# Performance work log

Measured on AMD Instinct MI355X. Metric: run time of the kernel, lower is better.

## Reference

```python
import jax, jax.numpy as jnp
import numpy as np
import math

N = 50000   # nodes
E = 800000  # edges
D = 64      # in_feat_dim == out_feat_dim
T = 8       # num node types
R = 8       # num relations
SQRT_DK = math.sqrt(D)


def typed_matmul(x, W, types, num_types):
    """Row-wise x[i] @ W[types[i]] without materializing [E, D, D] gathered weights."""
    out = jnp.zeros((x.shape[0], W.shape[-1]), x.dtype)
    for t in range(num_types):
        out = out + jnp.where((types == t)[:, None], x @ W[t], 0.0)
    return out


def segment_softmax(score, index, num_segments):
    smax = jax.ops.segment_max(score, index, num_segments=num_segments)
    ex = jnp.exp(score - smax[index])
    ssum = jax.ops.segment_sum(ex, index, num_segments=num_segments)
    return ex / (ssum[index] + 1e-16)


def setup_inputs() -> dict:
    key = jax.random.key(0)
    ks = jax.random.split(key, 10)
    h = jax.random.normal(ks[0], (N, D), dtype=jnp.float32)
    adj = jax.random.randint(ks[1], (2, E), 0, N, dtype=jnp.int64)
    edge_type = jax.random.randint(ks[2], (E,), 0, R, dtype=jnp.int64)
    node_type = jax.random.randint(ks[3], (N,), 0, T, dtype=jnp.int64)
    k_weights = jax.random.uniform(ks[4], (T, D, D), dtype=jnp.float32)
    q_weights = jax.random.uniform(ks[5], (T, D, D), dtype=jnp.float32)
    v_weights = jax.random.uniform(ks[6], (T, D, D), dtype=jnp.float32)
    a_weights = jax.random.uniform(ks[7], (T, D, D), dtype=jnp.float32)
    relation_att = jax.random.uniform(ks[8], (R, D, D), dtype=jnp.float32)
    relation_msg = jax.random.uniform(ks[9], (R, D, D), dtype=jnp.float32)
    relation_pri = jnp.ones((R, 1), dtype=jnp.float32)
    skip = jnp.ones((T,), dtype=jnp.float32)
    return {
        "h": h, "adj": adj, "edge_type": edge_type, "node_type": node_type,
        "src_type": 0, "dst_type": 0,
        "k_weights": k_weights, "q_weights": q_weights, "v_weights": v_weights,
        "a_weights": a_weights, "relation_pri": relation_pri,
        "relation_att": relation_att, "relation_msg": relation_msg, "skip": skip,
    }


def reference(h, adj, edge_type, node_type, src_type, dst_type,
              k_weights, q_weights, v_weights, a_weights,
              relation_pri, relation_att, relation_msg, skip):
    src = adj[0]  # _j side (messages come from src)
    dst = adj[1]  # _i side (scatter/softmax index)

    # Node-type-indexed projections (done per node, then gathered per edge --
    # identical math to the per-edge bmm in the original).
    k_node = typed_matmul(h, k_weights, node_type, T)  # [N, D]
    q_node = typed_matmul(h, q_weights, node_type, T)
    v_node = typed_matmul(h, v_weights, node_type, T)

    # Relation-indexed per-edge transforms.
    k = typed_matmul(k_node[src], relation_att, edge_type, R)  # [E, D]
    v = typed_matmul(v_node[src], relation_msg, edge_type, R)  # [E, D]
    q = q_node[dst]                                            # [E, D]

    attn_score = jnp.sum(k * q, axis=1, keepdims=True) * relation_pri[edge_type] / SQRT_DK  # [E, 1]
    alpha = segment_softmax(attn_score, dst, N)  # edge softmax over incoming edges
    rst = v * alpha                              # [E, D]

    agg = jax.ops.segment_sum(rst, dst, num_segments=N)  # [N, D]

    # Update: node-type-indexed output transform scaled by sigmoid(skip[type]).
    trans_out = typed_matmul(agg, a_weights, node_type, T)
    alpha_skip = jax.nn.sigmoid(skip[node_type])
    return trans_out * alpha_skip[:, None]
```

## Files before the change

### kernel.cpp

```cpp
#include <hip/hip_runtime.h>
#include <math.h>

typedef float f32x4 __attribute__((ext_vector_type(4)));
typedef short bf16x8 __attribute__((ext_vector_type(8)));
typedef _Float16 f16x8 __attribute__((ext_vector_type(8)));
typedef _Float16 f16x4 __attribute__((ext_vector_type(4)));

#define D 64
#define TT 8
#define RR 8

#define SCAN_TPB 256
#define SCAN_CH 4
#define SCAN_ELEMS (SCAN_TPB * SCAN_CH)

#define HIST_CH 8
#define SCAT_CH 4
#define SCORE_XB 256
#define V2_XB 64
#define AGG_XB 256

__device__ __forceinline__ float bf2f(unsigned short u) {
    union { unsigned int i; float f; } x;
    x.i = ((unsigned int)u) << 16;
    return x.f;
}
__device__ __forceinline__ unsigned short f2bf(float f) {
    union { float f; unsigned int i; } x;
    x.f = f;
    unsigned int i = x.i;
    unsigned int r = (i + 0x7FFFu + ((i >> 16) & 1u)) >> 16;
    return (unsigned short)r;
}
struct BfPair { short hi; short lo; };
__device__ __forceinline__ BfPair split2(float x) {
    BfPair p;
    unsigned short h = f2bf(x);
    p.hi = (short)h;
    p.lo = (short)f2bf(x - bf2f(h));
    return p;
}
__device__ __forceinline__ void load_A_split(const float* __restrict__ p, bf16x8& ah, bf16x8& al) {
#pragma unroll
    for (int i = 0; i < 8; ++i) {
        BfPair s = split2(p[i]);
        ah[i] = s.hi; al[i] = s.lo;
    }
}
__device__ __forceinline__ void load_B_split(const float* __restrict__ W, int ks, int c, int lane,
                                             bf16x8& bh, bf16x8& bl) {
    int n = lane & 15, q = lane >> 4;
#pragma unroll
    for (int i = 0; i < 8; ++i) {
        BfPair s = split2(W[(ks * 32 + q * 8 + i) * 64 + c * 16 + n]);
        bh[i] = s.hi; bl[i] = s.lo;
    }
}
__device__ __forceinline__ void load_B_split_f16(const float* __restrict__ W, int ks, int c, int lane,
                                                 f16x8& bh, f16x8& bl) {
    int n = lane & 15, q = lane >> 4;
#pragma unroll
    for (int i = 0; i < 8; ++i) {
        float w = W[(ks * 32 + q * 8 + i) * 64 + c * 16 + n];
        _Float16 h = (_Float16)w;
        bh[i] = h;
        bl[i] = (_Float16)(w - (float)h);
    }
}
__device__ __forceinline__ f16x8 load_B_frag_f16(const float* __restrict__ W, int ks, int c, int lane) {
    int n = lane & 15, q = lane >> 4;
    f16x8 r;
#pragma unroll
    for (int i = 0; i < 8; ++i)
        r[i] = (_Float16)W[(ks * 32 + q * 8 + i) * 64 + c * 16 + n];
    return r;
}

#define MFMA16(a, b, c) __builtin_amdgcn_mfma_f32_16x16x32_bf16(a, b, c, 0, 0, 0)
#define MFMAH(a, b, c)  __builtin_amdgcn_mfma_f32_16x16x32_f16(a, b, c, 0, 0, 0)

#define SPLIT_MFMA_BODY(acc, A0h, A0l, A1h, A1l, Bh, Bl)          \
    _Pragma("unroll")                                             \
    for (int c = 0; c < 4; ++c) {                                 \
        acc[c] = MFMA16(A0h, Bh[0][c], acc[c]);                   \
        acc[c] = MFMA16(A0l, Bh[0][c], acc[c]);                   \
        acc[c] = MFMA16(A0h, Bl[0][c], acc[c]);                   \
        acc[c] = MFMA16(A1h, Bh[1][c], acc[c]);                   \
        acc[c] = MFMA16(A1l, Bh[1][c], acc[c]);                   \
        acc[c] = MFMA16(A1h, Bl[1][c], acc[c]);                   \
    }

__global__ void hist_kernel(const int* __restrict__ dst, const int* __restrict__ et,
                            const int* __restrict__ nt,
                            int* __restrict__ deg, int* __restrict__ tcnt, int* __restrict__ rcnt,
                            int* __restrict__ erank, int N, int E) {
    __shared__ int l_r[RR], l_t[TT];
    if (threadIdx.x < RR) l_r[threadIdx.x] = 0;
    if (threadIdx.x < TT) l_t[threadIdx.x] = 0;
    __syncthreads();
    const int stride = gridDim.x * blockDim.x;
    const int tid = blockIdx.x * blockDim.x + threadIdx.x;
#pragma unroll
    for (int i = 0; i < HIST_CH; ++i) {
        int e = tid + i * stride;
        if (e < E) {
            erank[e] = atomicAdd(&deg[dst[e]], 1);
            atomicAdd(&l_r[et[e]], 1);
        }
    }
#pragma unroll
    for (int i = 0; i < HIST_CH; ++i) {
        int n = tid + i * stride;
        if (n < N) atomicAdd(&l_t[nt[n]], 1);
    }
    __syncthreads();
    if (threadIdx.x < RR && l_r[threadIdx.x]) atomicAdd(&rcnt[threadIdx.x], l_r[threadIdx.x]);
    if (threadIdx.x < TT && l_t[threadIdx.x]) atomicAdd(&tcnt[threadIdx.x], l_t[threadIdx.x]);
}

__global__ void scan_sum_kernel(const int* __restrict__ deg, int* __restrict__ bsum, int N) {
    __shared__ int ws[SCAN_TPB / 64];
    int tid = threadIdx.x;
    int base = blockIdx.x * SCAN_ELEMS + tid * SCAN_CH;
    int s = 0;
#pragma unroll
    for (int i = 0; i < SCAN_CH; ++i) {
        int idx = base + i;
        if (idx < N) s += deg[idx];
    }
#pragma unroll
    for (int d = 32; d; d >>= 1) s += __shfl_xor(s, d, 64);
    if ((tid & 63) == 0) ws[tid >> 6] = s;
    __syncthreads();
    if (tid == 0) {
        int t = 0;
#pragma unroll
        for (int i = 0; i < SCAN_TPB / 64; ++i) t += ws[i];
        bsum[blockIdx.x] = t;
    }
}
__global__ void scan_out_kernel(const int* __restrict__ deg, const int* __restrict__ bsum, int nsb,
                                int* __restrict__ off, int N, int Etot,
                                const int* __restrict__ tcnt, int* __restrict__ toff, int* __restrict__ tcur,
                                const int* __restrict__ rcnt, int* __restrict__ roff, int* __restrict__ rcur) {
    __shared__ int ts[SCAN_TPB];
    __shared__ int bb;
    int tid = threadIdx.x;
    if (tid < 64) {
        int v = 0;
        if (nsb <= 64) {
            v = (tid < nsb && tid < blockIdx.x) ? bsum[tid] : 0;
#pragma unroll
            for (int d = 32; d; d >>= 1) v += __shfl_xor(v, d, 64);
        } else if (tid == 0) {
            for (int b = 0; b < blockIdx.x; ++b) v += bsum[b];
        }
        if (tid == 0) bb = v;
    }
    if (blockIdx.x == 0 && tid == 1) {
        int a = 0;
        for (int t = 0; t < TT; ++t) { toff[t] = a; tcur[t] = a; a += tcnt[t]; }
        toff[TT] = a;
        int b2 = 0;
        for (int r = 0; r < RR; ++r) { roff[r] = b2; rcur[r] = b2; b2 += rcnt[r]; }
        roff[RR] = b2;
        off[N] = Etot;
    }
    int base = blockIdx.x * SCAN_ELEMS + tid * SCAN_CH;
    int loc[SCAN_CH];
    int s = 0;
#pragma unroll
    for (int i = 0; i < SCAN_CH; ++i) {
        int idx = base + i;
        int v = (idx < N) ? deg[idx] : 0;
        loc[i] = v; s += v;
    }
    ts[tid] = s;
    __syncthreads();
    for (int sh = 1; sh < SCAN_TPB; sh <<= 1) {
        int v = (tid >= sh) ? ts[tid - sh] : 0;
        __syncthreads();
        ts[tid] += v;
        __syncthreads();
    }
    int run = bb + ((tid > 0) ? ts[tid - 1] : 0);
#pragma unroll
    for (int i = 0; i < SCAN_CH; ++i) {
        int idx = base + i;
        if (idx < N) { off[idx] = run; run += loc[i]; }
    }
}

__global__ void scatter_kernel(const int* __restrict__ src, const int* __restrict__ dst,
                               const int* __restrict__ et, const int* __restrict__ nt,
                               const int* __restrict__ offs, const int* __restrict__ erank,
                               int* __restrict__ tcur, int* __restrict__ rcur,
                               int* __restrict__ rsrc, int* __restrict__ rdst,
                               int* __restrict__ rdpos, int* __restrict__ nidx, int N, int E) {
    __shared__ int l_r[RR], l_t[TT], base_r[RR], base_t[TT];
    if (threadIdx.x < RR) l_r[threadIdx.x] = 0;
    if (threadIdx.x < TT) l_t[threadIdx.x] = 0;
    __syncthreads();
    const int stride = gridDim.x * blockDim.x;
    const int tid = blockIdx.x * blockDim.x + threadIdx.x;
    int s[SCAT_CH], d[SCAT_CH], r[SCAT_CH], rrank[SCAT_CH];
    int t[SCAT_CH], trank[SCAT_CH];
#pragma unroll
    for (int i = 0; i < SCAT_CH; ++i) {
        int e = tid + i * stride;
        if (e < E) {
            s[i] = src[e]; d[i] = dst[e]; r[i] = et[e];
            rrank[i] = atomicAdd(&l_r[r[i]], 1);
        }
        int n = tid + i * stride;
        if (n < N) {
            t[i] = nt[n];
            trank[i] = atomicAdd(&l_t[t[i]], 1);
        }
    }
    __syncthreads();
    if (threadIdx.x < RR)
        base_r[threadIdx.x] = l_r[threadIdx.x] ? atomicAdd(&rcur[threadIdx.x], l_r[threadIdx.x]) : 0;
    if (threadIdx.x < TT)
        base_t[threadIdx.x] = l_t[threadIdx.x] ? atomicAdd(&tcur[threadIdx.x], l_t[threadIdx.x]) : 0;
    __syncthreads();
#pragma unroll
    for (int i = 0; i < SCAT_CH; ++i) {
        int e = tid + i * stride;
        if (e < E) {
            int pos = offs[d[i]] + erank[e];
            int rp = base_r[r[i]] + rrank[i];
            rsrc[rp] = s[i]; rdst[rp] = d[i]; rdpos[rp] = pos;
        }
        int n = tid + i * stride;
        if (n < N) nidx[base_t[t[i]] + trank[i]] = n;
    }
}

__global__ void proj_kernel(const float* __restrict__ h,
                            const float* __restrict__ Wk, const float* __restrict__ Wq,
                            const float* __restrict__ Wv,
                            const int* __restrict__ toff, const int* __restrict__ nidx,
                            _Float16* __restrict__ kh16,
                            _Float16* __restrict__ qout, _Float16* __restrict__ vout) {
    const int t = blockIdx.z, a = blockIdx.y, lane = threadIdx.x;
    const int beg = toff[t], end = toff[t + 1], cnt = end - beg;
    if (cnt <= 0) return;
    const int nstrips = (cnt + 15) >> 4;
    const float* W = (a == 0 ? Wk : (a == 1 ? Wq : Wv)) + (size_t)t * 4096;
    const int m = lane & 15, quad = lane >> 4;

    bf16x8 Bh[2][4], Bl[2][4];
#pragma unroll
    for (int ks = 0; ks < 2; ++ks)
#pragma unroll
        for (int c = 0; c < 4; ++c) load_B_split(W, ks, c, lane, Bh[ks][c], Bl[ks][c]);

    _Float16* out = (a == 0) ? kh16 : (a == 1 ? qout : vout);

    for (int s = blockIdx.x; s < nstrips; s += gridDim.x) {
        int base = beg + s * 16;
        int rA = base + m; if (rA > end - 1) rA = end - 1;
        const float* hp = h + (size_t)nidx[rA] * D;
        bf16x8 A0h, A0l, A1h, A1l;
        load_A_split(hp + quad * 8, A0h, A0l);
        load_A_split(hp + 32 + quad * 8, A1h, A1l);
        f32x4 acc[4];
#pragma unroll
        for (int c = 0; c < 4; ++c) acc[c] = (f32x4){0.f, 0.f, 0.f, 0.f};
        SPLIT_MFMA_BODY(acc, A0h, A0l, A1h, A1l, Bh, Bl)
#pragma unroll
        for (int reg = 0; reg < 4; ++reg) {
            int rr = base + quad * 4 + reg;
            if (rr < end) {
                int nid = nidx[rr];
#pragma unroll
                for (int c = 0; c < 4; ++c)
                    out[(size_t)nid * D + c * 16 + m] = (_Float16)acc[c][reg];
            }
        }
    }
}

__global__ void score_v2_kernel(const int* __restrict__ rsrc, const int* __restrict__ rdst,
                                const int* __restrict__ rdpos, const int* __restrict__ roff,
                                const _Float16* __restrict__ kh16,
                                const _Float16* __restrict__ qn, const float* __restrict__ Aatt,
                                const float* __restrict__ pri, int2* __restrict__ rec,
                                const _Float16* __restrict__ vn, const float* __restrict__ Amsg,
                                _Float16* __restrict__ V2, int N) {
    const int r = blockIdx.y;
    const int lane = threadIdx.x & 63;
    const int wv = threadIdx.x >> 6;
    const int m = lane & 15, quad = lane >> 4;

    if (blockIdx.x >= SCORE_XB) {
        const int g = (blockIdx.x - SCORE_XB) * 4 + wv;
        const int nstrips = (N + 15) >> 4;
        const float* W = Amsg + (size_t)r * 4096;
        f16x8 B[2][4];
#pragma unroll
        for (int ks = 0; ks < 2; ++ks)
#pragma unroll
            for (int c = 0; c < 4; ++c) B[ks][c] = load_B_frag_f16(W, ks, c, lane);

        for (int s = g; s < nstrips; s += V2_XB * 4) {
            int base = s * 16;
            int rA = base + m; if (rA > N - 1) rA = N - 1;
            f16x8 A0 = *(const f16x8*)(vn + (size_t)rA * D + quad * 8);
            f16x8 A1 = *(const f16x8*)(vn + (size_t)rA * D + 32 + quad * 8);
            f32x4 acc[4];
#pragma unroll
            for (int c = 0; c < 4; ++c) acc[c] = (f32x4){0.f, 0.f, 0.f, 0.f};
#pragma unroll
            for (int c = 0; c < 4; ++c) {
                acc[c] = MFMAH(A0, B[0][c], acc[c]);
                acc[c] = MFMAH(A1, B[1][c], acc[c]);
            }
#pragma unroll
            for (int reg = 0; reg < 4; ++reg) {
                int rr = base + quad * 4 + reg;
                if (rr < N) {
#pragma unroll
                    for (int c = 0; c < 4; ++c)
                        V2[((size_t)rr * RR + r) * D + c * 16 + m] = (_Float16)acc[c][reg];
                }
            }
        }
        return;
    }

    const int beg = roff[r], end = roff[r + 1], cnt = end - beg;
    if (cnt <= 0) return;
    const int nstrips = (cnt + 15) >> 4;
    const float scale = pri[r] * 0.125f;
    const float* W = Aatt + (size_t)r * 4096;

    f16x8 Bh[2][4], Bl[2][4];
#pragma unroll
    for (int ks = 0; ks < 2; ++ks)
#pragma unroll
        for (int c = 0; c < 4; ++c) load_B_split_f16(W, ks, c, lane, Bh[ks][c], Bl[ks][c]);

    const int g = blockIdx.x * 4 + wv;
    for (int st = g; st < nstrips; st += SCORE_XB * 4) {
        int base = st * 16;
        int ia = base + m; if (ia > cnt - 1) ia = cnt - 1;
        int s = rsrc[beg + ia];
        const _Float16* kr = kh16 + (size_t)s * D;
        f16x8 A0 = *(const f16x8*)(kr + quad * 8);
        f16x8 A1 = *(const f16x8*)(kr + 32 + quad * 8);
        f32x4 acc[4];
#pragma unroll
        for (int c = 0; c < 4; ++c) acc[c] = (f32x4){0.f, 0.f, 0.f, 0.f};
#pragma unroll
        for (int c = 0; c < 4; ++c) {
            acc[c] = MFMAH(A0, Bh[0][c], acc[c]);
            acc[c] = MFMAH(A0, Bl[0][c], acc[c]);
            acc[c] = MFMAH(A1, Bh[1][c], acc[c]);
            acc[c] = MFMAH(A1, Bl[1][c], acc[c]);
        }

        float p4[4];
#pragma unroll
        for (int reg = 0; reg < 4; ++reg) {
            int ie = base + quad * 4 + reg; if (ie > cnt - 1) ie = cnt - 1;
            const _Float16* qp = qn + (size_t)rdst[beg + ie] * D + m;
            float pr = acc[0][reg] * (float)qp[0] + acc[1][reg] * (float)qp[16]
                     + acc[2][reg] * (float)qp[32] + acc[3][reg] * (float)qp[48];
#pragma unroll
            for (int d = 8; d; d >>= 1) pr += __shfl_xor(pr, d, 64);
            p4[reg] = pr;
        }
        if (m < 4) {
            int idx = base + quad * 4 + m;
            if (idx < cnt) {
                float v = (m == 0) ? p4[0] : (m == 1) ? p4[1] : (m == 2) ? p4[2] : p4[3];
                int sagain = rsrc[beg + idx];
                int2 rc;
                rc.x = __float_as_int(v * scale);
                rc.y = (sagain << 3) | r;
                rec[rdpos[beg + idx]] = rc;
            }
        }
    }
}

__global__ void agg_out_kernel(const int* __restrict__ offs, const int2* __restrict__ rec,
                               const _Float16* __restrict__ V2,
                               const float* __restrict__ Wa, const float* __restrict__ skp,
                               const int* __restrict__ toff, const int* __restrict__ nidx,
                               float* __restrict__ out) {
    const int t = blockIdx.y;
    const int beg = toff[t], end = toff[t + 1], cnt = end - beg;
    if (cnt <= 0) return;
    const int nstrips = (cnt + 15) >> 4;
    const int lane = threadIdx.x & 63;
    const int wv = threadIdx.x >> 6;
    const int quad = lane >> 4, ql = lane & 15;
    const int q16 = wv * 4 + quad;
    const int qb = quad << 4;
    const int m = lane & 15, qd = lane >> 4;
    const float sg = 1.f / (1.f + __expf(-skp[t]));

    __shared__ float As[16][68];

    bf16x8 Bh2[2], Bl2[2];
    const float* W = Wa + (size_t)t * 4096;
#pragma unroll
    for (int ks = 0; ks < 2; ++ks) load_B_split(W, ks, wv, lane, Bh2[ks], Bl2[ks]);

    for (int s = blockIdx.x; s < nstrips; s += gridDim.x) {
        int base = beg + s * 16;
        int rr = base + q16; if (rr > end - 1) rr = end - 1;
        int i = nidx[rr];
        const int ebeg = offs[i], eend = offs[i + 1];
        float mmax = -INFINITY, lsum = 0.f;
        float a0 = 0.f, a1 = 0.f, a2 = 0.f, a3 = 0.f;
        for (int cs = ebeg; cs < eend; cs += 16) {
            int cl = eend - cs; if (cl > 16) cl = 16;
            int2 rc; rc.y = 0;
            float sc = -INFINITY;
            if (ql < cl) { rc = rec[cs + ql]; sc = __int_as_float(rc.x); }
            float cm = sc;
#pragma unroll
            for (int d = 8; d; d >>= 1) cm = fmaxf(cm, __shfl_xor(cm, d, 64));
            float mn = fmaxf(mmax, cm);
            float cf = __expf(mmax - mn);
            float ex = (ql < cl) ? __expf(sc - mn) : 0.f;
            float csum = ex;
#pragma unroll
            for (int d = 8; d; d >>= 1) csum += __shfl_xor(csum, d, 64);
            lsum = lsum * cf + csum;
            a0 *= cf; a1 *= cf; a2 *= cf; a3 *= cf;
            for (int e = 0; e < cl; e += 4) {
                float w0 = __shfl(ex, qb + e, 64),     w1 = __shfl(ex, qb + e + 1, 64);
                float w2 = __shfl(ex, qb + e + 2, 64), w3 = __shfl(ex, qb + e + 3, 64);
                int   i0 = __shfl(rc.y, qb + e, 64),     i1 = __shfl(rc.y, qb + e + 1, 64);
                int   i2 = __shfl(rc.y, qb + e + 2, 64), i3 = __shfl(rc.y, qb + e + 3, 64);
                f16x4 v0 = *(const f16x4*)(V2 + (size_t)i0 * D + ql * 4);
                f16x4 v1 = *(const f16x4*)(V2 + (size_t)i1 * D + ql * 4);
                f16x4 v2 = *(const f16x4*)(V2 + (size_t)i2 * D + ql * 4);
                f16x4 v3 = *(const f16x4*)(V2 + (size_t)i3 * D + ql * 4);
                a0 += w0 * (float)v0[0] + w1 * (float)v1[0] + w2 * (float)v2[0] + w3 * (float)v3[0];
                a1 += w0 * (float)v0[1] + w1 * (float)v1[1] + w2 * (float)v2[1] + w3 * (float)v3[1];
                a2 += w0 * (float)v0[2] + w1 * (float)v1[2] + w2 * (float)v2[2] + w3 * (float)v3[2];
                a3 += w0 * (float)v0[3] + w1 * (float)v1[3] + w2 * (float)v2[3] + w3 * (float)v3[3];
            }
            mmax = mn;
        }
        float inv = 1.f / (lsum + 1e-16f);
        As[q16][ql * 4 + 0] = a0 * inv;
        As[q16][ql * 4 + 1] = a1 * inv;
        As[q16][ql * 4 + 2] = a2 * inv;
        As[q16][ql * 4 + 3] = a3 * inv;
        __syncthreads();

        bf16x8 A0h, A0l, A1h, A1l;
        load_A_split(&As[m][qd * 8], A0h, A0l);
        load_A_split(&As[m][32 + qd * 8], A1h, A1l);
        f32x4 acc = (f32x4){0.f, 0.f, 0.f, 0.f};
        acc = MFMA16(A0h, Bh2[0], acc);
        acc = MFMA16(A0l, Bh2[0], acc);
        acc = MFMA16(A0h, Bl2[0], acc);
        acc = MFMA16(A1h, Bh2[1], acc);
        acc = MFMA16(A1l, Bh2[1], acc);
        acc = MFMA16(A1h, Bl2[1], acc);
#pragma unroll
        for (int reg = 0; reg < 4; ++reg) {
            int rrr = base + qd * 4 + reg;
            if (rrr < end)
                out[(size_t)nidx[rrr] * D + wv * 16 + m] = acc[reg] * sg;
        }
        __syncthreads();
    }
}

extern "C" void kernel_launch(void* const* d_in, const int* in_sizes, int n_in,
                              void* d_out, int out_size, void* d_ws, size_t ws_size,
                              hipStream_t stream) {
    const float* h     = (const float*)d_in[0];
    const int*   adj   = (const int*)d_in[1];
    const int*   etype = (const int*)d_in[2];
    const int*   ntype = (const int*)d_in[3];
    const float* Wk    = (const float*)d_in[6];
    const float* Wq    = (const float*)d_in[7];
    const float* Wv    = (const float*)d_in[8];
    const float* Wa    = (const float*)d_in[9];
    const float* pri   = (const float*)d_in[10];
    const float* Aatt  = (const float*)d_in[11];
    const float* Amsg  = (const float*)d_in[12];
    const float* skp   = (const float*)d_in[13];
    const int N = in_sizes[3];
    const int E = in_sizes[2];
    float* out = (float*)d_out;

    char* w = (char*)d_ws;
    auto alloc = [&](size_t b) { char* p = w; w += (b + 255) & ~(size_t)255; return p; };
    _Float16* kh16 = (_Float16*)alloc((size_t)N * D * 2);
    _Float16* qn   = (_Float16*)alloc((size_t)N * D * 2);
    _Float16* vn   = (_Float16*)alloc((size_t)N * D * 2);
    _Float16* V2   = (_Float16*)alloc((size_t)N * RR * D * 2);
    int* deg  = (int*)alloc((size_t)(N + 16) * 4);
    int* tcnt = deg + N;
    int* rcnt = deg + N + 8;
    int* offs = (int*)alloc((size_t)(N + 1) * 4);
    int* erank = (int*)alloc((size_t)E * 4);
    int* toff = (int*)alloc(64);
    int* tcur = (int*)alloc(64);
    int* roff = (int*)alloc(64);
    int* rcur = (int*)alloc(64);
    int2* rec = (int2*)alloc((size_t)E * 8);
    int* rsrc  = (int*)alloc((size_t)E * 4);
    int* rdst  = (int*)alloc((size_t)E * 4);
    int* rdpos = (int*)alloc((size_t)E * 4);
    int* nidx  = (int*)alloc((size_t)N * 4);
    const int nsb = (N + SCAN_ELEMS - 1) / SCAN_ELEMS;
    int* bsum  = (int*)alloc((size_t)nsb * 4);

    (void)hipMemsetAsync(deg, 0, (size_t)(N + 16) * 4, stream);

    const int mx = (E > N ? E : N);
    const int histBlocks = (mx + 256 * HIST_CH - 1) / (256 * HIST_CH);
    hist_kernel<<<histBlocks, 256, 0, stream>>>(adj + E, etype, ntype, deg, tcnt, rcnt, erank, N, E);
    scan_sum_kernel<<<nsb, SCAN_TPB, 0, stream>>>(deg, bsum, N);
    scan_out_kernel<<<nsb, SCAN_TPB, 0, stream>>>(deg, bsum, nsb, offs, N, E,
                                                  tcnt, toff, tcur, rcnt, roff, rcur);
    const int scatBlocks = (mx + 256 * SCAT_CH - 1) / (256 * SCAT_CH);
    scatter_kernel<<<scatBlocks, 256, 0, stream>>>(adj, adj + E, etype, ntype,
                                                   offs, erank, tcur, rcur,
                                                   rsrc, rdst, rdpos, nidx, N, E);
    proj_kernel<<<dim3(128, 3, TT), 64, 0, stream>>>(h, Wk, Wq, Wv, toff, nidx, kh16, qn, vn);
    score_v2_kernel<<<dim3(SCORE_XB + V2_XB, RR), 256, 0, stream>>>(rsrc, rdst, rdpos, roff,
                                                                    kh16, qn, Aatt, pri, rec,
                                                                    vn, Amsg, V2, N);
    agg_out_kernel<<<dim3(AGG_XB, TT), 256, 0, stream>>>(offs, rec, V2, Wa, skp, toff, nidx, out);
}
```

Measured before the change: 257.9 us.

## Bucket relation-sorted edges by destination block for locality in score kernel

Replaces the per-relation counting sort of edges with a finer (relation, destination-block of 64 nodes) bucket histogram. The bucket counts are appended to the degree array and scanned together, so edges within each relation come out roughly sorted by destination. The score kernel switches from strided strip assignment to contiguous chunks per wave to exploit that locality when gathering q rows and writing records. The cost is more global atomics (one per edge into bucket counters in both hist and scatter, instead of shared-memory atomics) and a larger scan.

```diff
diff --git a/kernel.cpp b/kernel.cpp
--- a/kernel.cpp
+++ b/kernel.cpp
@@ -19,6 +19,8 @@
 #define SCORE_XB 256
 #define V2_XB 64
 #define AGG_XB 256
+
+#define DBSHIFT 6
 
 __device__ __forceinline__ float bf2f(unsigned short u) {
     union { unsigned int i; float f; } x;
@@ -92,10 +94,9 @@
 
 __global__ void hist_kernel(const int* __restrict__ dst, const int* __restrict__ et,
                             const int* __restrict__ nt,
-                            int* __restrict__ deg, int* __restrict__ tcnt, int* __restrict__ rcnt,
-                            int* __restrict__ erank, int N, int E) {
-    __shared__ int l_r[RR], l_t[TT];
-    if (threadIdx.x < RR) l_r[threadIdx.x] = 0;
+                            int* __restrict__ degb, int* __restrict__ tcnt,
+                            int* __restrict__ erank, int N, int E, int NBR) {
+    __shared__ int l_t[TT];
     if (threadIdx.x < TT) l_t[threadIdx.x] = 0;
     __syncthreads();
     const int stride = gridDim.x * blockDim.x;
@@ -104,8 +105,9 @@
     for (int i = 0; i < HIST_CH; ++i) {
         int e = tid + i * stride;
         if (e < E) {
-            erank[e] = atomicAdd(&deg[dst[e]], 1);
-            atomicAdd(&l_r[et[e]], 1);
+            int d = dst[e];
+            erank[e] = atomicAdd(&degb[d], 1);
+            atomicAdd(&degb[N + et[e] * NBR + (d >> DBSHIFT)], 1);
         }
     }
 #pragma unroll
@@ -114,7 +116,6 @@
         if (n < N) atomicAdd(&l_t[nt[n]], 1);
     }
     __syncthreads();
-    if (threadIdx.x < RR && l_r[threadIdx.x]) atomicAdd(&rcnt[threadIdx.x], l_r[threadIdx.x]);
     if (threadIdx.x < TT && l_t[threadIdx.x]) atomicAdd(&tcnt[threadIdx.x], l_t[threadIdx.x]);
 }
 
@@ -141,8 +142,7 @@
 }
 __global__ void scan_out_kernel(const int* __restrict__ deg, const int* __restrict__ bsum, int nsb,
                                 int* __restrict__ off, int N, int Etot,
-                                const int* __restrict__ tcnt, int* __restrict__ toff, int* __restrict__ tcur,
-                                const int* __restrict__ rcnt, int* __restrict__ roff, int* __restrict__ rcur) {
+                                const int* __restrict__ tcnt, int* __restrict__ toff, int* __restrict__ tcur) {
     __shared__ int ts[SCAN_TPB];
     __shared__ int bb;
     int tid = threadIdx.x;
@@ -161,9 +161,6 @@
         int a = 0;
         for (int t = 0; t < TT; ++t) { toff[t] = a; tcur[t] = a; a += tcnt[t]; }
         toff[TT] = a;
-        int b2 = 0;
-        for (int r = 0; r < RR; ++r) { roff[r] = b2; rcur[r] = b2; b2 += rcnt[r]; }
-        roff[RR] = b2;
         off[N] = Etot;
     }
     int base = blockIdx.x * SCAN_ELEMS + tid * SCAN_CH;
@@ -194,23 +191,22 @@
 __global__ void scatter_kernel(const int* __restrict__ src, const int* __restrict__ dst,
                                const int* __restrict__ et, const int* __restrict__ nt,
                                const int* __restrict__ offs, const int* __restrict__ erank,
-                               int* __restrict__ tcur, int* __restrict__ rcur,
+                               int* __restrict__ tcur, int* __restrict__ bcur,
                                int* __restrict__ rsrc, int* __restrict__ rdst,
-                               int* __restrict__ rdpos, int* __restrict__ nidx, int N, int E) {
-    __shared__ int l_r[RR], l_t[TT], base_r[RR], base_t[TT];
-    if (threadIdx.x < RR) l_r[threadIdx.x] = 0;
+                               int* __restrict__ rdpos, int* __restrict__ nidx,
+                               int N, int E, int NBR) {
+    __shared__ int l_t[TT], base_t[TT];
     if (threadIdx.x < TT) l_t[threadIdx.x] = 0;
     __syncthreads();
     const int stride = gridDim.x * blockDim.x;
     const int tid = blockIdx.x * blockDim.x + threadIdx.x;
-    int s[SCAT_CH], d[SCAT_CH], r[SCAT_CH], rrank[SCAT_CH];
+    int s[SCAT_CH], d[SCAT_CH], r[SCAT_CH];
     int t[SCAT_CH], trank[SCAT_CH];
 #pragma unroll
     for (int i = 0; i < SCAT_CH; ++i) {
         int e = tid + i * stride;
         if (e < E) {
             s[i] = src[e]; d[i] = dst[e]; r[i] = et[e];
-            rrank[i] = atomicAdd(&l_r[r[i]], 1);
         }
         int n = tid + i * stride;
         if (n < N) {
@@ -219,8 +215,6 @@
         }
     }
     __syncthreads();
-    if (threadIdx.x < RR)
-        base_r[threadIdx.x] = l_r[threadIdx.x] ? atomicAdd(&rcur[threadIdx.x], l_r[threadIdx.x]) : 0;
     if (threadIdx.x < TT)
         base_t[threadIdx.x] = l_t[threadIdx.x] ? atomicAdd(&tcur[threadIdx.x], l_t[threadIdx.x]) : 0;
     __syncthreads();
@@ -228,8 +222,9 @@
     for (int i = 0; i < SCAT_CH; ++i) {
         int e = tid + i * stride;
         if (e < E) {
+            int bucket = r[i] * NBR + (d[i] >> DBSHIFT);
+            int rp = (offs[N + bucket] - E) + atomicAdd(&bcur[bucket], 1);
             int pos = offs[d[i]] + erank[e];
-            int rp = base_r[r[i]] + rrank[i];
             rsrc[rp] = s[i]; rdst[rp] = d[i]; rdpos[rp] = pos;
         }
         int n = tid + i * stride;
@@ -283,12 +278,12 @@
 }
 
 __global__ void score_v2_kernel(const int* __restrict__ rsrc, const int* __restrict__ rdst,
-                                const int* __restrict__ rdpos, const int* __restrict__ roff,
+                                const int* __restrict__ rdpos, const int* __restrict__ offs,
                                 const _Float16* __restrict__ kh16,
                                 const _Float16* __restrict__ qn, const float* __restrict__ Aatt,
                                 const float* __restrict__ pri, int2* __restrict__ rec,
                                 const _Float16* __restrict__ vn, const float* __restrict__ Amsg,
-                                _Float16* __restrict__ V2, int N) {
+                                _Float16* __restrict__ V2, int N, int NBR) {
     const int r = blockIdx.y;
     const int lane = threadIdx.x & 63;
     const int wv = threadIdx.x >> 6;
@@ -330,7 +325,10 @@
         return;
     }
 
-    const int beg = roff[r], end = roff[r + 1], cnt = end - beg;
+    const int base0 = offs[N];
+    const int beg = offs[N + r * NBR] - base0;
+    const int end = offs[N + (r + 1) * NBR] - base0;
+    const int cnt = end - beg;
     if (cnt <= 0) return;
     const int nstrips = (cnt + 15) >> 4;
     const float scale = pri[r] * 0.125f;
@@ -343,7 +341,11 @@
         for (int c = 0; c < 4; ++c) load_B_split_f16(W, ks, c, lane, Bh[ks][c], Bl[ks][c]);
 
     const int g = blockIdx.x * 4 + wv;
-    for (int st = g; st < nstrips; st += SCORE_XB * 4) {
+    const int nw = SCORE_XB * 4;
+    const int chunk = (nstrips + nw - 1) / nw;
+    int st0 = g * chunk;
+    int st1 = st0 + chunk; if (st1 > nstrips) st1 = nstrips;
+    for (int st = st0; st < st1; ++st) {
         int base = st * 16;
         int ia = base + m; if (ia > cnt - 1) ia = cnt - 1;
         int s = rsrc[beg + ia];
@@ -495,44 +497,46 @@
     const int E = in_sizes[2];
     float* out = (float*)d_out;
 
+    const int NBR = (N + 63) >> DBSHIFT;
+    const int NB  = RR * NBR;
+    const int Nscan = N + NB;
+
     char* w = (char*)d_ws;
     auto alloc = [&](size_t b) { char* p = w; w += (b + 255) & ~(size_t)255; return p; };
     _Float16* kh16 = (_Float16*)alloc((size_t)N * D * 2);
     _Float16* qn   = (_Float16*)alloc((size_t)N * D * 2);
     _Float16* vn   = (_Float16*)alloc((size_t)N * D * 2);
     _Float16* V2   = (_Float16*)alloc((size_t)N * RR * D * 2);
-    int* deg  = (int*)alloc((size_t)(N + 16) * 4);
-    int* tcnt = deg + N;
-    int* rcnt = deg + N + 8;
-    int* offs = (int*)alloc((size_t)(N + 1) * 4);
+    int* degb = (int*)alloc((size_t)(Nscan + 8 + NB) * 4);
+    int* tcnt = degb + Nscan;
+    int* bcur = tcnt + 8;
+    int* offs = (int*)alloc((size_t)(Nscan + 1) * 4);
     int* erank = (int*)alloc((size_t)E * 4);
     int* toff = (int*)alloc(64);
     int* tcur = (int*)alloc(64);
-    int* roff = (int*)alloc(64);
-    int* rcur = (int*)alloc(64);
     int2* rec = (int2*)alloc((size_t)E * 8);
     int* rsrc  = (int*)alloc((size_t)E * 4);
     int* rdst  = (int*)alloc((size_t)E * 4);
     int* rdpos = (int*)alloc((size_t)E * 4);
     int* nidx  = (int*)alloc((size_t)N * 4);
-    const int nsb = (N + SCAN_ELEMS - 1) / SCAN_ELEMS;
+    const int nsb = (Nscan + SCAN_ELEMS - 1) / SCAN_ELEMS;
     int* bsum  = (int*)alloc((size_t)nsb * 4);
 
-    (void)hipMemsetAsync(deg, 0, (size_t)(N + 16) * 4, stream);
+    (void)hipMemsetAsync(degb, 0, (size_t)(Nscan + 8 + NB) * 4, stream);
 
     const int mx = (E > N ? E : N);
     const int histBlocks = (mx + 256 * HIST_CH - 1) / (256 * HIST_CH);
-    hist_kernel<<<histBlocks, 256, 0, stream>>>(adj + E, etype, ntype, deg, tcnt, rcnt, erank, N, E);
-    scan_sum_kernel<<<nsb, SCAN_TPB, 0, stream>>>(deg, bsum, N);
-    scan_out_kernel<<<nsb, SCAN_TPB, 0, stream>>>(deg, bsum, nsb, offs, N, E,
-                                                  tcnt, toff, tcur, rcnt, roff, rcur);
+    hist_kernel<<<histBlocks, 256, 0, stream>>>(adj + E, etype, ntype, degb, tcnt, erank, N, E, NBR);
+    scan_sum_kernel<<<nsb, SCAN_TPB, 0, stream>>>(degb, bsum, Nscan);
+    scan_out_kernel<<<nsb, SCAN_TPB, 0, stream>>>(degb, bsum, nsb, offs, Nscan, 2 * E,
+                                                  tcnt, toff, tcur);
     const int scatBlocks = (mx + 256 * SCAT_CH - 1) / (256 * SCAT_CH);
     scatter_kernel<<<scatBlocks, 256, 0, stream>>>(adj, adj + E, etype, ntype,
-                                                   offs, erank, tcur, rcur,
-                                                   rsrc, rdst, rdpos, nidx, N, E);
+                                                   offs, erank, tcur, bcur,
+                                                   rsrc, rdst, rdpos, nidx, N, E, NBR);
     proj_kernel<<<dim3(128, 3, TT), 64, 0, stream>>>(h, Wk, Wq, Wv, toff, nidx, kh16, qn, vn);
-    score_v2_kernel<<<dim3(SCORE_XB + V2_XB, RR), 256, 0, stream>>>(rsrc, rdst, rdpos, roff,
+    score_v2_kernel<<<dim3(SCORE_XB + V2_XB, RR), 256, 0, stream>>>(rsrc, rdst, rdpos, offs,
                                                                     kh16, qn, Aatt, pri, rec,
-                                                                    vn, Amsg, V2, N);
+                                                                    vn, Amsg, V2, N, NBR);
     agg_out_kernel<<<dim3(AGG_XB, TT), 256, 0, stream>>>(offs, rec, V2, Wa, skp, toff, nidx, out);
 }
```

Result: slower. 328.1 us (+27.2%).

## Prefetch next strip indices and K rows in score kernel, vectorize f16 stores

Applied to the files above, without the earlier changes.

Permutes the output column mapping of the B fragments so each lane owns 4 contiguous columns. This lets the projection and V2 kernels write one f16x4 per row instead of four scattered halves, and lets the score kernel read q as one f16x4. The score loop is software-pipelined: it prefetches source, destination and position indices two strips ahead and the K rows one strip ahead. Edge indices are then passed between lanes with shuffles instead of being reloaded. This hides gather latency at the cost of more registers.

```diff
diff --git a/kernel.cpp b/kernel.cpp
--- a/kernel.cpp
+++ b/kernel.cpp
@@ -56,12 +56,21 @@
         bh[i] = s.hi; bl[i] = s.lo;
     }
 }
+__device__ __forceinline__ void load_B_splitp(const float* __restrict__ W, int ks, int c, int lane,
+                                              bf16x8& bh, bf16x8& bl) {
+    int n = lane & 15, q = lane >> 4;
+#pragma unroll
+    for (int i = 0; i < 8; ++i) {
+        BfPair s = split2(W[(ks * 32 + q * 8 + i) * 64 + n * 4 + c]);
+        bh[i] = s.hi; bl[i] = s.lo;
+    }
+}
 __device__ __forceinline__ void load_B_split_f16(const float* __restrict__ W, int ks, int c, int lane,
                                                  f16x8& bh, f16x8& bl) {
     int n = lane & 15, q = lane >> 4;
 #pragma unroll
     for (int i = 0; i < 8; ++i) {
-        float w = W[(ks * 32 + q * 8 + i) * 64 + c * 16 + n];
+        float w = W[(ks * 32 + q * 8 + i) * 64 + n * 4 + c];
         _Float16 h = (_Float16)w;
         bh[i] = h;
         bl[i] = (_Float16)(w - (float)h);
@@ -72,7 +81,7 @@
     f16x8 r;
 #pragma unroll
     for (int i = 0; i < 8; ++i)
-        r[i] = (_Float16)W[(ks * 32 + q * 8 + i) * 64 + c * 16 + n];
+        r[i] = (_Float16)W[(ks * 32 + q * 8 + i) * 64 + n * 4 + c];
     return r;
 }
 
@@ -254,7 +263,7 @@
 #pragma unroll
     for (int ks = 0; ks < 2; ++ks)
 #pragma unroll
-        for (int c = 0; c < 4; ++c) load_B_split(W, ks, c, lane, Bh[ks][c], Bl[ks][c]);
+        for (int c = 0; c < 4; ++c) load_B_splitp(W, ks, c, lane, Bh[ks][c], Bl[ks][c]);
 
     _Float16* out = (a == 0) ? kh16 : (a == 1 ? qout : vout);
 
@@ -274,9 +283,10 @@
             int rr = base + quad * 4 + reg;
             if (rr < end) {
                 int nid = nidx[rr];
-#pragma unroll
-                for (int c = 0; c < 4; ++c)
-                    out[(size_t)nid * D + c * 16 + m] = (_Float16)acc[c][reg];
+                f16x4 o;
+#pragma unroll
+                for (int c = 0; c < 4; ++c) o[c] = (_Float16)acc[c][reg];
+                *(f16x4*)(out + (size_t)nid * D + m * 4) = o;
             }
         }
     }
@@ -321,9 +331,10 @@
             for (int reg = 0; reg < 4; ++reg) {
                 int rr = base + quad * 4 + reg;
                 if (rr < N) {
-#pragma unroll
-                    for (int c = 0; c < 4; ++c)
-                        V2[((size_t)rr * RR + r) * D + c * 16 + m] = (_Float16)acc[c][reg];
+                    f16x4 o;
+#pragma unroll
+                    for (int c = 0; c < 4; ++c) o[c] = (_Float16)acc[c][reg];
+                    *(f16x4*)(V2 + ((size_t)rr * RR + r) * D + m * 4) = o;
                 }
             }
         }
@@ -342,14 +353,28 @@
 #pragma unroll
         for (int c = 0; c < 4; ++c) load_B_split_f16(W, ks, c, lane, Bh[ks][c], Bl[ks][c]);
 
+    const int NW = SCORE_XB * 4;
     const int g = blockIdx.x * 4 + wv;
-    for (int st = g; st < nstrips; st += SCORE_XB * 4) {
-        int base = st * 16;
-        int ia = base + m; if (ia > cnt - 1) ia = cnt - 1;
-        int s = rsrc[beg + ia];
-        const _Float16* kr = kh16 + (size_t)s * D;
-        f16x8 A0 = *(const f16x8*)(kr + quad * 8);
-        f16x8 A1 = *(const f16x8*)(kr + 32 + quad * 8);
+    if (g >= nstrips) return;
+
+    int sC, dC, pC, sN = 0, dN = 0, pN = 0;
+    f16x8 A0, A1;
+    {
+        int ia = g * 16 + m; if (ia > cnt - 1) ia = cnt - 1;
+        sC = rsrc[beg + ia]; dC = rdst[beg + ia]; pC = rdpos[beg + ia];
+    }
+    {
+        const _Float16* kr = kh16 + (size_t)sC * D;
+        A0 = *(const f16x8*)(kr + quad * 8);
+        A1 = *(const f16x8*)(kr + 32 + quad * 8);
+    }
+    if (g + NW < nstrips) {
+        int ia = (g + NW) * 16 + m; if (ia > cnt - 1) ia = cnt - 1;
+        sN = rsrc[beg + ia]; dN = rdst[beg + ia]; pN = rdpos[beg + ia];
+    }
+
+    for (int st = g; st < nstrips; st += NW) {
+        const int base = st * 16;
         f32x4 acc[4];
 #pragma unroll
         for (int c = 0; c < 4; ++c) acc[c] = (f32x4){0.f, 0.f, 0.f, 0.f};
@@ -361,27 +386,47 @@
             acc[c] = MFMAH(A1, Bl[1][c], acc[c]);
         }
 
+        const bool hN = (st + NW) < nstrips;
+        f16x8 A0n, A1n;
+        if (hN) {
+            const _Float16* kr = kh16 + (size_t)sN * D;
+            A0n = *(const f16x8*)(kr + quad * 8);
+            A1n = *(const f16x8*)(kr + 32 + quad * 8);
+        }
+        int sNN = 0, dNN = 0, pNN = 0;
+        const bool hNN = (st + 2 * NW) < nstrips;
+        if (hNN) {
+            int ia = (st + 2 * NW) * 16 + m; if (ia > cnt - 1) ia = cnt - 1;
+            sNN = rsrc[beg + ia]; dNN = rdst[beg + ia]; pNN = rdpos[beg + ia];
+        }
+
         float p4[4];
 #pragma unroll
         for (int reg = 0; reg < 4; ++reg) {
-            int ie = base + quad * 4 + reg; if (ie > cnt - 1) ie = cnt - 1;
-            const _Float16* qp = qn + (size_t)rdst[beg + ie] * D + m;
-            float pr = acc[0][reg] * (float)qp[0] + acc[1][reg] * (float)qp[16]
-                     + acc[2][reg] * (float)qp[32] + acc[3][reg] * (float)qp[48];
+            int dd = __shfl(dC, quad * 4 + reg, 64);
+            f16x4 q4 = *(const f16x4*)(qn + (size_t)dd * D + m * 4);
+            float pr = acc[0][reg] * (float)q4[0] + acc[1][reg] * (float)q4[1]
+                     + acc[2][reg] * (float)q4[2] + acc[3][reg] * (float)q4[3];
 #pragma unroll
             for (int d = 8; d; d >>= 1) pr += __shfl_xor(pr, d, 64);
             p4[reg] = pr;
         }
+        int wsrc = __shfl(sC, quad * 4 + (m & 3), 64);
+        int wpos = __shfl(pC, quad * 4 + (m & 3), 64);
+        float wval = ((m & 3) == 0) ? p4[0] : ((m & 3) == 1) ? p4[1] : ((m & 3) == 2) ? p4[2] : p4[3];
         if (m < 4) {
             int idx = base + quad * 4 + m;
             if (idx < cnt) {
-                float v = (m == 0) ? p4[0] : (m == 1) ? p4[1] : (m == 2) ? p4[2] : p4[3];
-                int sagain = rsrc[beg + idx];
                 int2 rc;
-                rc.x = __float_as_int(v * scale);
-                rc.y = (sagain << 3) | r;
-                rec[rdpos[beg + idx]] = rc;
+                rc.x = __float_as_int(wval * scale);
+                rc.y = (wsrc << 3) | r;
+                rec[wpos] = rc;
             }
+        }
+        if (hN) {
+            A0 = A0n; A1 = A1n;
+            sC = sN; dC = dN; pC = pN;
+            sN = sNN; dN = dNN; pN = pNN;
         }
     }
 }
```

Result: no change. 256.2 us (-0.7%).
